# Kernel optimization log

Hardware: AMD Instinct MI355X
Metric: run time of the kernel (lower is better)

Reference implementation:

```python
import jax, jax.numpy as jnp
import numpy as np
import math

H = 12      # num_heads
DH = 64     # head_dim
NEG = -1e30 # masked logit value
M_TRUNC = 2 # poisson_trunc


def _rotate_half(x):
    d = x.shape[-1] // 2
    return jnp.concatenate([-x[..., d:], x[..., :d]], axis=-1)


def setup_inputs() -> dict:
    key = jax.random.key(0)
    k0, k1, k2 = jax.random.split(key, 3)
    B, T, C = 1, 4096, 768
    x = jax.random.normal(k0, (B, T, C), jnp.float32)
    W_qkv = jax.random.normal(k1, (C, 3 * C), jnp.float32) * (C ** -0.5)
    W_proj = jax.random.normal(k2, (C, C), jnp.float32) * (C ** -0.5)
    # standard RoPE tables, concat layout matching rotate_half
    inv_freq = 1.0 / (10000.0 ** (jnp.arange(0, DH, 2, dtype=jnp.float32) / DH))
    ang = jnp.arange(T, dtype=jnp.float32)[:, None] * inv_freq[None, :]  # [T, DH/2]
    cos = jnp.concatenate([jnp.cos(ang), jnp.cos(ang)], axis=-1)  # [T, DH]
    sin = jnp.concatenate([jnp.sin(ang), jnp.sin(ang)], axis=-1)
    dt_logit = jnp.float32(math.log(0.999 / (1.0 - 0.999)))            # sigmoid -> 0.999
    kappa_uncon = jnp.float32(math.log(math.expm1(1.0) + 1e-8))        # softplus -> 1.0
    xi_uncon = jnp.float32(math.log(math.expm1(32.0) + 1e-8))          # softplus -> 32.0
    return dict(x=x, cos=cos, sin=sin, W_qkv=W_qkv, W_proj=W_proj,
                dt_logit=dt_logit, kappa_uncon=kappa_uncon, xi_uncon=xi_uncon)


def reference(x, cos, sin, W_qkv, W_proj, dt_logit, kappa_uncon, xi_uncon):
    B, T, C = x.shape
    qkv = x @ W_qkv                         # [B,T,3C]
    q, k, v = jnp.split(qkv, 3, axis=-1)
    split_heads = lambda t: t.reshape(B, T, H, DH).transpose(0, 2, 1, 3)  # [B,H,T,Dh]
    q, k, v = split_heads(q), split_heads(k), split_heads(v)
    c, s = cos[None, None], sin[None, None]
    q = q * c + _rotate_half(q) * s
    k = k * c + _rotate_half(k) * s
    dp = jnp.einsum('bhtd,bhsd->bhts', q, k) / math.sqrt(DH)  # [B,H,T,T]
    kappa = jax.nn.softplus(kappa_uncon)
    xi = jax.nn.softplus(xi_uncon)
    idx = jnp.arange(T)
    dist = (idx[:, None] - idx[None, :]).astype(jnp.float32)
    prior = -kappa * (dist / xi) ** 2       # Gaussian diffusion prior
    allowed = idx[:, None] >= idx[None, :]  # causal tril
    logits = jnp.where(allowed[None, None], dp + prior[None, None], NEG)
    P = jax.nn.softmax(logits, axis=-1)     # row-stochastic Markov kernel
    # truncated, renormalized Poisson mixture of matrix powers: exp(t(P-I)) v
    dt = jax.nn.sigmoid(dt_logit)
    w = jnp.stack([dt ** m * jnp.exp(-dt) / math.factorial(m) for m in range(M_TRUNC + 1)])
    w = w / jnp.sum(w)
    y = w[0] * v
    pv = v
    for m in range(1, M_TRUNC + 1):         # fixed small iteration count
        pv = jnp.einsum('bhts,bhsd->bhtd', P, pv)
        y = y + w[m] * pv
    y = y.transpose(0, 2, 1, 3).reshape(B, T, C)
    return y @ W_proj
```

## Files before the change

### kernel.cpp

```cpp
#include <hip/hip_runtime.h>
#include <hip/hip_bf16.h>

#define Tn 4096
#define Cn 768
#define Hn 12
#define DHn 64
#define BAND 192
#define QBLK 64
#define TJ 256
#define NTW 13

typedef __attribute__((ext_vector_type(8))) short short8;
typedef __attribute__((ext_vector_type(4))) short short4v;
typedef __attribute__((ext_vector_type(4))) float f32x4;

__device__ __forceinline__ float b2f(unsigned short u) {
  union { unsigned int i; float f; } z; z.i = ((unsigned int)u) << 16; return z.f;
}
__device__ __forceinline__ unsigned short f2b(float f) {
  union { float f; unsigned int i; } z; z.f = f;
  unsigned int r = z.i + 0x7FFFu + ((z.i >> 16) & 1u);
  return (unsigned short)(r >> 16);
}

__global__ __launch_bounds__(256) void k_prep(const float* __restrict__ x,
                                              unsigned short* __restrict__ x_bf,
                                              const float* __restrict__ Wqkv,
                                              unsigned short* __restrict__ WqkvT,
                                              const float* __restrict__ Wproj,
                                              unsigned short* __restrict__ WprojT) {
  __shared__ float tile[32][33];
  int b = blockIdx.x, tid = threadIdx.x;
  if (b < 512) {
    int n4 = Tn * Cn / 4;
    for (int i = b * 256 + tid; i < n4; i += 512 * 256) {
      float4 v = ((const float4*)x)[i];
      short4v o;
      o.x = (short)f2b(v.x); o.y = (short)f2b(v.y);
      o.z = (short)f2b(v.z); o.w = (short)f2b(v.w);
      ((short4v*)x_bf)[i] = o;
    }
    return;
  }
  const float* W; unsigned short* WT; int N, r;
  if (b < 2240) { r = b - 512; W = Wqkv; WT = WqkvT; N = 3 * Cn; }
  else          { r = b - 2240; W = Wproj; WT = WprojT; N = Cn; }
  int nb = N / 32;
  int n0 = (r % nb) * 32, k0 = (r / nb) * 32;
  int tx = tid & 31, ty = tid >> 5;
  for (int rr = ty; rr < 32; rr += 8) tile[rr][tx] = W[(size_t)(k0 + rr) * N + n0 + tx];
  __syncthreads();
  for (int rr = ty; rr < 32; rr += 8) WT[(size_t)(n0 + rr) * Cn + k0 + tx] = f2b(tile[tx][rr]);
}


__device__ __forceinline__ void g_stage(const unsigned short* __restrict__ Ab,
                                        const unsigned short* __restrict__ Bb,
                                        int K, unsigned short* buf, int kt, int tid) {
  int k0 = kt << 5;
#pragma unroll
  for (int it = 0; it < 2; ++it) {
    int c = it * 256 + tid;
    int row = c >> 2;
    int kc = (c & 3) ^ (row & 3);
    const unsigned short* ga = Ab + (size_t)row * K + k0 + kc * 8;
    __builtin_amdgcn_global_load_lds((const __attribute__((address_space(1))) void*)ga,
                                     (__attribute__((address_space(3))) void*)(buf + c * 8),
                                     16, 0, 0);
  }
#pragma unroll
  for (int it = 0; it < 2; ++it) {
    int c = it * 256 + tid;
    int row = c >> 2;
    int kc = (c & 3) ^ (row & 3);
    const unsigned short* gb = Bb + (size_t)row * K + k0 + kc * 8;
    __builtin_amdgcn_global_load_lds((const __attribute__((address_space(1))) void*)gb,
                                     (__attribute__((address_space(3))) void*)(buf + 4096 + c * 8),
                                     16, 0, 0);
  }
}

#define GEMM_MAIN(K_)                                                                     \
  __shared__ __align__(16) unsigned short Ls[2][8192];                                    \
  int tid = threadIdx.x, lane = tid & 63, wave = tid >> 6;                                \
  int lq = lane & 15, g = (lane >> 4) & 3;                                                \
  int wr = wave >> 1, wc = wave & 1;                                                      \
  int nx = gridDim.x;                                                                     \
  int nwg = nx * gridDim.y;                                                               \
  int lid = blockIdx.y * nx + blockIdx.x;                                                 \
  int swz = (lid & 7) * (nwg >> 3) + (lid >> 3);                                          \
  int bx = swz % nx, by = swz / nx;                                                       \
  int m0 = by * 128, n0 = bx * 128;                                                       \
  const unsigned short* Ab = A + (size_t)m0 * (K_);                                       \
  const unsigned short* Bb = BT + (size_t)n0 * (K_);                                      \
  f32x4 acc[4][4] = {};                                                                   \
  const int NK = (K_) >> 5;                                                               \
  g_stage(Ab, Bb, (K_), Ls[0], 0, tid);                                                   \
  g_stage(Ab, Bb, (K_), Ls[1], 1, tid);                                                   \
  for (int kt = 0; kt < NK; ++kt) {                                                       \
    if (kt + 1 < NK) asm volatile("s_waitcnt vmcnt(4)" ::: "memory");                     \
    else             asm volatile("s_waitcnt vmcnt(0)" ::: "memory");                     \
    __builtin_amdgcn_s_barrier();                                                         \
    __builtin_amdgcn_sched_barrier(0);                                                    \
    const unsigned short* Ac = Ls[kt & 1];                                                \
    const unsigned short* Bc = Ls[kt & 1] + 4096;                                         \
    short8 a[4], b[4];                                                                    \
    _Pragma("unroll")                                                                     \
    for (int m = 0; m < 4; ++m) {                                                         \
      int row = wr * 64 + m * 16 + lq;                                                    \
      int s = g ^ (row & 3);                                                              \
      a[m] = *(const short8*)(Ac + row * 32 + s * 8);                                     \
    }                                                                                     \
    _Pragma("unroll")                                                                     \
    for (int n = 0; n < 4; ++n) {                                                         \
      int row = wc * 64 + n * 16 + lq;                                                    \
      int s = g ^ (row & 3);                                                              \
      b[n] = *(const short8*)(Bc + row * 32 + s * 8);                                     \
    }                                                                                     \
    __builtin_amdgcn_s_setprio(1);                                                        \
    _Pragma("unroll")                                                                     \
    for (int m = 0; m < 4; ++m)                                                           \
      _Pragma("unroll")                                                                   \
      for (int n = 0; n < 4; ++n)                                                         \
        acc[m][n] = __builtin_amdgcn_mfma_f32_16x16x32_bf16(a[m], b[n], acc[m][n], 0, 0, 0); \
    __builtin_amdgcn_s_setprio(0);                                                        \
    __builtin_amdgcn_sched_barrier(0);                                                    \
    __builtin_amdgcn_s_barrier();                                                         \
    if (kt + 2 < NK) g_stage(Ab, Bb, (K_), Ls[kt & 1], kt + 2, tid);                      \
  }

__global__ __launch_bounds__(256, 4) void k_gqkv(const unsigned short* __restrict__ A,
                                                 const unsigned short* __restrict__ BT,
                                                 const float* __restrict__ cosT,
                                                 const float* __restrict__ sinT,
                                                 unsigned short* __restrict__ qout,
                                                 unsigned short* __restrict__ kout,
                                                 unsigned short* __restrict__ vout) {
  GEMM_MAIN(Cn)
  int col0 = n0 + wc * 64;
  int part = col0 / Cn;
  unsigned short* Lo = (unsigned short*)Ls;
#pragma unroll
  for (int m = 0; m < 4; ++m)
#pragma unroll
    for (int i = 0; i < 4; ++i) {
      int lr = wr * 64 + m * 16 + g * 4 + i;
      int t = m0 + lr;
#pragma unroll
      for (int n = 0; n < 4; ++n) {
        int d = n * 16 + lq;
        float val = acc[m][n][i];
        if (part < 2) {
          float cv = cosT[t * DHn + d], sv = sinT[t * DHn + d];
          float partner = acc[m][n ^ 2][i];
          val = (n < 2) ? fmaf(-partner, sv, val * cv) : fmaf(partner, sv, val * cv);
        }
        Lo[lr * 128 + wc * 64 + d] = f2b(val);
      }
    }
  __syncthreads();
#pragma unroll
  for (int it = 0; it < 8; ++it) {
    int c = it * 256 + tid;
    int tr = c >> 4, cc = c & 15;
    int cola = n0 + (cc << 3);
    int pp = cola / Cn;
    int h = (cola % Cn) / DHn;
    int d0 = cola % DHn;
    unsigned short* dst = pp == 0 ? qout : (pp == 1 ? kout : vout);
    *(short8*)(dst + ((size_t)h * Tn + (m0 + tr)) * DHn + d0) = *(const short8*)(Lo + tr * 128 + (cc << 3));
  }
}

__global__ __launch_bounds__(256, 4) void k_gproj(const unsigned short* __restrict__ A,
                                                  const unsigned short* __restrict__ BT,
                                                  float* __restrict__ Cout) {
  GEMM_MAIN(Cn)
  int r0 = m0 + wr * 64 + g * 4;
  int c0 = n0 + wc * 64 + lq;
#pragma unroll
  for (int m = 0; m < 4; ++m)
#pragma unroll
    for (int n = 0; n < 4; ++n)
#pragma unroll
      for (int i = 0; i < 4; ++i)
        Cout[(size_t)(r0 + m * 16 + i) * Cn + c0 + n * 16] = acc[m][n][i];
}

__device__ __forceinline__ void stage_subtiled(const unsigned short* __restrict__ srcHead,
                                               int jt0, unsigned short* lds, int tid, int wave) {
#pragma unroll
  for (int it = 0; it < 8; ++it) {
    int c = it * 256 + tid;
    int j = jt0 + ((c >> 5) << 2) + ((c & 7) >> 1);
    j = j < 0 ? 0 : j;
    int d0 = (((c >> 3) & 3) << 4) + ((c & 1) << 3);
    const unsigned short* ga = srcHead + (size_t)j * DHn + d0;
    __builtin_amdgcn_global_load_lds((const __attribute__((address_space(1))) void*)ga,
                                     (__attribute__((address_space(3))) void*)(lds + (it * 4 + wave) * 512),
                                     16, 0, 0);
  }
}

__device__ __forceinline__ void pv_tr(const unsigned short* Vt, const short8* af,
                                      int wave, int lane, f32x4* oacc) {
  int lq = lane & 15, g = lane >> 4;
  unsigned base = (unsigned)(size_t)(const __attribute__((address_space(3))) unsigned short*)Vt;
  unsigned pl = base + lq * 8;
#pragma unroll
  for (int e = 0; e < 7; ++e) {
    int kl = 16 * wave + 32 * e + 8 * g;
    if (kl > TJ - 8) kl = TJ - 8;
    unsigned pe = pl + kl * 128;
    unsigned long long rr[8];
#pragma unroll
    for (int dt = 0; dt < 4; ++dt) {
      asm volatile("ds_read_b64_tr_b16 %0, %1" : "=v"(rr[2 * dt]) : "v"(pe + dt * 128));
      asm volatile("ds_read_b64_tr_b16 %0, %1" : "=v"(rr[2 * dt + 1]) : "v"(pe + dt * 128 + 512));
    }
    asm volatile("s_waitcnt lgkmcnt(0)");
    __builtin_amdgcn_sched_barrier(0);
#pragma unroll
    for (int dt = 0; dt < 4; ++dt) {
      union { unsigned long long u[2]; short8 s; } vb;
      vb.u[0] = rr[2 * dt]; vb.u[1] = rr[2 * dt + 1];
      oacc[dt] = __builtin_amdgcn_mfma_f32_16x16x32_bf16(af[e], vb.s, oacc[dt], 0, 0, 0);
    }
  }
}

__global__ __launch_bounds__(256) void k_attn_a(const unsigned short* __restrict__ qr,
                                                const unsigned short* __restrict__ kr,
                                                const unsigned short* __restrict__ vin,
                                                unsigned short* __restrict__ pv1out,
                                                unsigned short* __restrict__ pfrag,
                                                const float* __restrict__ kap_p,
                                                const float* __restrict__ xi_p) {
  __shared__ unsigned short Ks[TJ * DHn];
  __shared__ unsigned short Vt[TJ * DHn];
  int tid = threadIdx.x, lane = tid & 63, wave = tid >> 6;
  int lq = lane & 15, g = lane >> 4;
  int i0 = blockIdx.x * QBLK, h = blockIdx.y;
  int jt0 = i0 - BAND;
  const size_t headoff = (size_t)h * Tn * DHn;

  const unsigned short* krh = kr + headoff;
#pragma unroll
  for (int it = 0; it < 8; ++it) {
    int u = it * 256 + tid;
    int row = u >> 3, c8 = u & 7;
    int j = jt0 + row; j = j < 0 ? 0 : j;
    const unsigned short* ga = krh + (size_t)j * DHn + ((c8 ^ (row & 7)) << 3);
    __builtin_amdgcn_global_load_lds((const __attribute__((address_space(1))) void*)ga,
                                     (__attribute__((address_space(3))) void*)((char*)Ks + (size_t)(it * 256 + wave * 64) * 16),
                                     16, 0, 0);
  }
  stage_subtiled(vin + headoff, jt0, Vt, tid, wave);

  const unsigned short* qrh = qr + headoff;
  int q0 = i0 + wave * 16;
  short8 qf0 = *(const short8*)(qrh + (size_t)(q0 + lq) * DHn + g * 8);
  short8 qf1 = *(const short8*)(qrh + (size_t)(q0 + lq) * DHn + 32 + g * 8);
  __syncthreads();

  f32x4 st[NTW];
#pragma unroll
  for (int t = 0; t < NTW; ++t) st[t] = (f32x4){0.f, 0.f, 0.f, 0.f};
#pragma unroll
  for (int t = 0; t < NTW; ++t) {
    int row = (wave + t) * 16 + lq;
    const char* kb = (const char*)Ks + row * 128;
    int sw = row & 7;
    short8 ka0 = *(const short8*)(kb + ((g ^ sw) << 4));
    short8 ka1 = *(const short8*)(kb + (((4 + g) ^ sw) << 4));
    st[t] = __builtin_amdgcn_mfma_f32_16x16x32_bf16(ka0, qf0, st[t], 0, 0, 0);
    st[t] = __builtin_amdgcn_mfma_f32_16x16x32_bf16(ka1, qf1, st[t], 0, 0, 0);
  }

  float kap = log1pf(__expf(*kap_p));
  float xi  = log1pf(__expf(*xi_p));
  const float LOG2E = 1.4426950408889634f;
  float sc = 0.125f * LOG2E;
  float c2 = kap / (xi * xi) * LOG2E;
  float db0 = (float)(lq + BAND - 4 * g);
  float jb0 = (float)(jt0 + 16 * wave + 4 * g);
  float m = -3.0e38f;
#pragma unroll
  for (int t = 0; t < NTW; ++t) {
#pragma unroll
    for (int r = 0; r < 4; ++r) {
      float off = (float)(16 * t + r);
      float dist = db0 - off;
      float jv = jb0 + off;
      float l2 = fmaf(dist * dist, -c2, st[t][r] * sc);
      bool bad = (dist < 0.f) || (jv < 0.f);
      l2 = bad ? -3.0e38f : l2;
      st[t][r] = l2;
      m = fmaxf(m, l2);
    }
  }
  m = fmaxf(m, __shfl_xor(m, 16));
  m = fmaxf(m, __shfl_xor(m, 32));
  float sum = 0.f;
#pragma unroll
  for (int t = 0; t < NTW; ++t) {
#pragma unroll
    for (int r = 0; r < 4; ++r) {
      float p = exp2f(st[t][r] - m);
      st[t][r] = p;
      sum += p;
    }
  }
  sum += __shfl_xor(sum, 16);
  sum += __shfl_xor(sum, 32);
  float inv_s = 1.f / sum;

  unsigned int pk0[NTW], pk1[NTW];
#pragma unroll
  for (int t = 0; t < NTW; ++t) {
    pk0[t] = (unsigned int)f2b(st[t][0] * inv_s) | ((unsigned int)f2b(st[t][1] * inv_s) << 16);
    pk1[t] = (unsigned int)f2b(st[t][2] * inv_s) | ((unsigned int)f2b(st[t][3] * inv_s) << 16);
  }

  short8 af[7];
  int srcA = lq + (g & 1) * 32;
  int srcB = srcA + 16;
  bool hiT = (g >= 2);
#pragma unroll
  for (int e = 0; e < 7; ++e) {
    unsigned int aA0 = __shfl(pk0[2 * e], srcA);
    unsigned int aA1 = __shfl(pk1[2 * e], srcA);
    unsigned int aB0 = __shfl(pk0[2 * e], srcB);
    unsigned int aB1 = __shfl(pk1[2 * e], srcB);
    unsigned int dw0, dw1, dw2, dw3;
    if (e < 6) {
      unsigned int bA0 = __shfl(pk0[2 * e + 1], srcA);
      unsigned int bA1 = __shfl(pk1[2 * e + 1], srcA);
      unsigned int bB0 = __shfl(pk0[2 * e + 1], srcB);
      unsigned int bB1 = __shfl(pk1[2 * e + 1], srcB);
      dw0 = hiT ? bA0 : aA0; dw1 = hiT ? bA1 : aA1;
      dw2 = hiT ? bB0 : aB0; dw3 = hiT ? bB1 : aB1;
    } else {
      dw0 = hiT ? 0u : aA0; dw1 = hiT ? 0u : aA1;
      dw2 = hiT ? 0u : aB0; dw3 = hiT ? 0u : aB1;
    }
    union { unsigned int u[4]; short8 s; } t2;
    t2.u[0] = dw0; t2.u[1] = dw1; t2.u[2] = dw2; t2.u[3] = dw3;
    af[e] = t2.s;
  }

  size_t pfb = ((((size_t)h * (Tn / QBLK) + blockIdx.x) * 4 + wave) * 7) * 512 + (size_t)lane * 8;
#pragma unroll
  for (int e = 0; e < 7; ++e)
    *(short8*)(pfrag + pfb + (size_t)e * 512) = af[e];

  f32x4 oacc[4];
#pragma unroll
  for (int dt = 0; dt < 4; ++dt) oacc[dt] = (f32x4){0.f, 0.f, 0.f, 0.f};
  pv_tr(Vt, af, wave, lane, oacc);

#pragma unroll
  for (int dt = 0; dt < 4; ++dt)
#pragma unroll
    for (int r = 0; r < 4; ++r) {
      int i = i0 + 16 * wave + 4 * g + r;
      pv1out[headoff + (size_t)i * DHn + dt * 16 + lq] = f2b(oacc[dt][r]);
    }
}

__global__ __launch_bounds__(256) void k_attn_b(const unsigned short* __restrict__ pv1,
                                                const unsigned short* __restrict__ v0,
                                                const unsigned short* __restrict__ pfrag,
                                                unsigned short* __restrict__ yout,
                                                const float* __restrict__ dt_logit_p) {
  __shared__ unsigned short Vt[TJ * DHn];
  int tid = threadIdx.x, lane = tid & 63, wave = tid >> 6;
  int lq = lane & 15, g = lane >> 4;
  int i0 = blockIdx.x * QBLK, h = blockIdx.y;
  int jt0 = i0 - BAND;
  const size_t headoff = (size_t)h * Tn * DHn;

  stage_subtiled(pv1 + headoff, jt0, Vt, tid, wave);

  short8 af[7];
  size_t pfb = ((((size_t)h * (Tn / QBLK) + blockIdx.x) * 4 + wave) * 7) * 512 + (size_t)lane * 8;
#pragma unroll
  for (int e = 0; e < 7; ++e)
    af[e] = *(const short8*)(pfrag + pfb + (size_t)e * 512);
  __syncthreads();

  f32x4 oacc[4];
#pragma unroll
  for (int dt = 0; dt < 4; ++dt) oacc[dt] = (f32x4){0.f, 0.f, 0.f, 0.f};
  pv_tr(Vt, af, wave, lane, oacc);

  float dtv = 1.f / (1.f + __expf(-*dt_logit_p));
  float a1 = dtv, a2 = 0.5f * dtv * dtv;
  float inv3 = 1.f / (1.f + a1 + a2);
  float w0 = inv3, w1 = a1 * inv3, w2 = a2 * inv3;

#pragma unroll
  for (int dt = 0; dt < 4; ++dt)
#pragma unroll
    for (int r = 0; r < 4; ++r) {
      int i = i0 + 16 * wave + 4 * g + r;
      int j = 192 + 16 * wave + 4 * g + r;
      unsigned boff = (unsigned)((j >> 2) * 512 + dt * 128 + (j & 3) * 32 + lq * 2);
      float p1 = b2f(*(const unsigned short*)((const char*)Vt + boff));
      float vv = b2f(v0[headoff + (size_t)i * DHn + dt * 16 + lq]);
      float yv = w0 * vv + w1 * p1 + w2 * oacc[dt][r];
      yout[(size_t)i * Cn + h * DHn + dt * 16 + lq] = f2b(yv);
    }
}

extern "C" void kernel_launch(void* const* d_in, const int* in_sizes, int n_in,
                              void* d_out, int out_size, void* d_ws, size_t ws_size,
                              hipStream_t stream) {
  (void)in_sizes; (void)n_in; (void)out_size; (void)ws_size;
  const float* x     = (const float*)d_in[0];
  const float* cosT  = (const float*)d_in[1];
  const float* sinT  = (const float*)d_in[2];
  const float* Wqkv  = (const float*)d_in[3];
  const float* Wproj = (const float*)d_in[4];
  const float* dtl   = (const float*)d_in[5];
  const float* kap   = (const float*)d_in[6];
  const float* xiu   = (const float*)d_in[7];
  float* out = (float*)d_out;
  char* ws = (char*)d_ws;
  size_t off = 0;
  auto alloc = [&](size_t bytes) { char* p = ws + off; off += (bytes + 255) & ~(size_t)255; return p; };
  unsigned short* x_bf   = (unsigned short*)alloc((size_t)Tn * Cn * 2);
  unsigned short* WqkvT  = (unsigned short*)alloc((size_t)3 * Cn * Cn * 2);
  unsigned short* WprojT = (unsigned short*)alloc((size_t)Cn * Cn * 2);
  unsigned short* q_r    = (unsigned short*)alloc((size_t)Hn * Tn * DHn * 2);
  unsigned short* k_r    = (unsigned short*)alloc((size_t)Hn * Tn * DHn * 2);
  unsigned short* v_s    = (unsigned short*)alloc((size_t)Hn * Tn * DHn * 2);
  unsigned short* pv1    = (unsigned short*)alloc((size_t)Hn * Tn * DHn * 2);
  unsigned short* y_bf   = (unsigned short*)alloc((size_t)Tn * Cn * 2);
  unsigned short* pfrag  = (unsigned short*)alloc((size_t)Hn * (Tn / QBLK) * 4 * 7 * 512 * 2);

  k_prep<<<2816, 256, 0, stream>>>(x, x_bf, Wqkv, WqkvT, Wproj, WprojT);
  k_gqkv<<<dim3(3 * Cn / 128, Tn / 128), 256, 0, stream>>>(
      x_bf, WqkvT, cosT, sinT, q_r, k_r, v_s);
  k_attn_a<<<dim3(Tn / QBLK, Hn), 256, 0, stream>>>(q_r, k_r, v_s, pv1, pfrag, kap, xiu);
  k_attn_b<<<dim3(Tn / QBLK, Hn), 256, 0, stream>>>(pv1, v_s, pfrag, y_bf, dtl);
  k_gproj<<<dim3(Cn / 128, Tn / 128), 256, 0, stream>>>(y_bf, WprojT, out);
}
```

Measured before the change: 90.46 us.

## Triple-buffer GEMM LDS staging with single barrier and new swizzle

The shared GEMM main loop goes from two LDS buffers to three. The prefetch for tile kt+2 is now issued right after the barrier, before compute, so the trailing barrier can be dropped and there is one barrier per k-step instead of two. The LDS layout packs two rows per 64-element line with an 8-way XOR swizzle to cut bank conflicts, and the setprio hints are removed. LDS use grows to 48KB per block, so launch bounds drop from 4 to 3 blocks per CU, and an extra __syncthreads is added before the QKV epilogue reuses LDS.

```diff
diff --git a/kernel.cpp b/kernel.cpp
--- a/kernel.cpp
+++ b/kernel.cpp
@@ -54,15 +54,17 @@
 }
 
 
-__device__ __forceinline__ void g_stage(const unsigned short* __restrict__ Ab,
-                                        const unsigned short* __restrict__ Bb,
-                                        int K, unsigned short* buf, int kt, int tid) {
+__device__ __forceinline__ void g_stage3(const unsigned short* __restrict__ Ab,
+                                         const unsigned short* __restrict__ Bb,
+                                         int K, unsigned short* buf, int kt, int tid) {
   int k0 = kt << 5;
 #pragma unroll
   for (int it = 0; it < 2; ++it) {
     int c = it * 256 + tid;
-    int row = c >> 2;
-    int kc = (c & 3) ^ (row & 3);
+    int jj = c >> 3, ss = c & 7;
+    int u = ss ^ (jj & 7);
+    int row = jj * 2 + (u >> 2);
+    int kc = u & 3;
     const unsigned short* ga = Ab + (size_t)row * K + k0 + kc * 8;
     __builtin_amdgcn_global_load_lds((const __attribute__((address_space(1))) void*)ga,
                                      (__attribute__((address_space(3))) void*)(buf + c * 8),
@@ -71,8 +73,10 @@
 #pragma unroll
   for (int it = 0; it < 2; ++it) {
     int c = it * 256 + tid;
-    int row = c >> 2;
-    int kc = (c & 3) ^ (row & 3);
+    int jj = c >> 3, ss = c & 7;
+    int u = ss ^ (jj & 7);
+    int row = jj * 2 + (u >> 2);
+    int kc = u & 3;
     const unsigned short* gb = Bb + (size_t)row * K + k0 + kc * 8;
     __builtin_amdgcn_global_load_lds((const __attribute__((address_space(1))) void*)gb,
                                      (__attribute__((address_space(3))) void*)(buf + 4096 + c * 8),
@@ -81,7 +85,7 @@
 }
 
 #define GEMM_MAIN(K_)                                                                     \
-  __shared__ __align__(16) unsigned short Ls[2][8192];                                    \
+  __shared__ __align__(16) unsigned short Ls[3][8192];                                    \
   int tid = threadIdx.x, lane = tid & 63, wave = tid >> 6;                                \
   int lq = lane & 15, g = (lane >> 4) & 3;                                                \
   int wr = wave >> 1, wc = wave & 1;                                                      \
@@ -95,41 +99,37 @@
   const unsigned short* Bb = BT + (size_t)n0 * (K_);                                      \
   f32x4 acc[4][4] = {};                                                                   \
   const int NK = (K_) >> 5;                                                               \
-  g_stage(Ab, Bb, (K_), Ls[0], 0, tid);                                                   \
-  g_stage(Ab, Bb, (K_), Ls[1], 1, tid);                                                   \
+  g_stage3(Ab, Bb, (K_), Ls[0], 0, tid);                                                  \
+  g_stage3(Ab, Bb, (K_), Ls[1], 1, tid);                                                  \
   for (int kt = 0; kt < NK; ++kt) {                                                       \
     if (kt + 1 < NK) asm volatile("s_waitcnt vmcnt(4)" ::: "memory");                     \
     else             asm volatile("s_waitcnt vmcnt(0)" ::: "memory");                     \
     __builtin_amdgcn_s_barrier();                                                         \
     __builtin_amdgcn_sched_barrier(0);                                                    \
-    const unsigned short* Ac = Ls[kt & 1];                                                \
-    const unsigned short* Bc = Ls[kt & 1] + 4096;                                         \
+    if (kt + 2 < NK) g_stage3(Ab, Bb, (K_), Ls[(kt + 2) % 3], kt + 2, tid);               \
+    const unsigned short* Ac = Ls[kt % 3];                                                \
+    const unsigned short* Bc = Ls[kt % 3] + 4096;                                         \
     short8 a[4], b[4];                                                                    \
     _Pragma("unroll")                                                                     \
     for (int m = 0; m < 4; ++m) {                                                         \
       int row = wr * 64 + m * 16 + lq;                                                    \
-      int s = g ^ (row & 3);                                                              \
-      a[m] = *(const short8*)(Ac + row * 32 + s * 8);                                     \
+      int s = (((row & 1) << 2) | g) ^ ((row >> 1) & 7);                                  \
+      a[m] = *(const short8*)(Ac + (row >> 1) * 64 + s * 8);                              \
     }                                                                                     \
     _Pragma("unroll")                                                                     \
     for (int n = 0; n < 4; ++n) {                                                         \
       int row = wc * 64 + n * 16 + lq;                                                    \
-      int s = g ^ (row & 3);                                                              \
-      b[n] = *(const short8*)(Bc + row * 32 + s * 8);                                     \
+      int s = (((row & 1) << 2) | g) ^ ((row >> 1) & 7);                                  \
+      b[n] = *(const short8*)(Bc + (row >> 1) * 64 + s * 8);                              \
     }                                                                                     \
-    __builtin_amdgcn_s_setprio(1);                                                        \
     _Pragma("unroll")                                                                     \
     for (int m = 0; m < 4; ++m)                                                           \
       _Pragma("unroll")                                                                   \
       for (int n = 0; n < 4; ++n)                                                         \
         acc[m][n] = __builtin_amdgcn_mfma_f32_16x16x32_bf16(a[m], b[n], acc[m][n], 0, 0, 0); \
-    __builtin_amdgcn_s_setprio(0);                                                        \
-    __builtin_amdgcn_sched_barrier(0);                                                    \
-    __builtin_amdgcn_s_barrier();                                                         \
-    if (kt + 2 < NK) g_stage(Ab, Bb, (K_), Ls[kt & 1], kt + 2, tid);                      \
-  }
-
-__global__ __launch_bounds__(256, 4) void k_gqkv(const unsigned short* __restrict__ A,
+  }
+
+__global__ __launch_bounds__(256, 3) void k_gqkv(const unsigned short* __restrict__ A,
                                                  const unsigned short* __restrict__ BT,
                                                  const float* __restrict__ cosT,
                                                  const float* __restrict__ sinT,
@@ -137,6 +137,7 @@
                                                  unsigned short* __restrict__ kout,
                                                  unsigned short* __restrict__ vout) {
   GEMM_MAIN(Cn)
+  __syncthreads();
   int col0 = n0 + wc * 64;
   int part = col0 / Cn;
   unsigned short* Lo = (unsigned short*)Ls;
@@ -172,7 +173,7 @@
   }
 }
 
-__global__ __launch_bounds__(256, 4) void k_gproj(const unsigned short* __restrict__ A,
+__global__ __launch_bounds__(256, 3) void k_gproj(const unsigned short* __restrict__ A,
                                                   const unsigned short* __restrict__ BT,
                                                   float* __restrict__ Cout) {
   GEMM_MAIN(Cn)
```

Result: no change. 88.75 us (-1.9%).
